# Optimization experiments

Hardware: AMD Instinct MI355X
Metric: run time of the kernel (lower is better)

Reference implementation:

```python
import jax, jax.numpy as jnp
import numpy as np

NUM_HEADS = 4
K_CLOSEST = 8
LN_EPS = 1e-5

B, N_REC, N_KP, F = 8, 4096, 20, 256


def setup_inputs() -> dict:
    key = jax.random.key(0)
    ks = jax.random.split(key, 5)
    h_rec = jax.random.normal(ks[0], (B, N_REC, F), dtype=jnp.float32)
    x_rec = jax.random.normal(ks[1], (B, N_REC, 3), dtype=jnp.float32) * 3.0
    h0_kp = jax.random.normal(ks[2], (B, N_KP, F), dtype=jnp.float32)
    # fc_src (shared for src and dst, bias=False): in_feats -> out_feats*num_heads
    W_src = jax.random.normal(ks[3], (F, F * NUM_HEADS), dtype=jnp.float32) / np.sqrt(F)
    # kp_feature_mlp: Linear(out_feats + k_closest, out_feats) + SiLU
    W_mlp = jax.random.normal(ks[4], (F + K_CLOSEST, F), dtype=jnp.float32) / np.sqrt(F + K_CLOSEST)
    b_mlp = jnp.zeros((F,), dtype=jnp.float32)
    ln_gamma = jnp.ones((F,), dtype=jnp.float32)
    ln_beta = jnp.zeros((F,), dtype=jnp.float32)
    return {"h_rec": h_rec, "x_rec": x_rec, "h0_kp": h0_kp, "W_src": W_src,
            "W_mlp": W_mlp, "b_mlp": b_mlp, "ln_gamma": ln_gamma, "ln_beta": ln_beta}


def reference(h_rec, x_rec, h0_kp, W_src, W_mlp, b_mlp, ln_gamma, ln_beta):
    Bb, Nr, Fd = h_rec.shape
    Nk = h0_kp.shape[1]
    H = NUM_HEADS
    D = W_src.shape[1] // H  # out_feats per head

    # fc_src applied to both rec and kp features (matches source, fc_dst unused)
    ft_src = (h_rec @ W_src).reshape(Bb, Nr, H, D)   # [B, Nr, H, D]
    ft_dst = (h0_kp @ W_src).reshape(Bb, Nk, H, D)   # [B, Nk, H, D]

    # per-edge dot-product scores over the complete bipartite rec->kp graph
    a = jnp.einsum('brhd,bkhd->brkh', ft_src, ft_dst) / jnp.sqrt(jnp.float32(D))
    a = jnp.exp(a)  # source uses plain exp (no max subtraction)
    sa = a / jnp.sum(a, axis=1, keepdims=True)        # segment softmax over rec atoms per kp

    # attention-weighted aggregation of rec positions, mean over heads
    agg = jnp.einsum('brkh,brc->bkhc', sa, x_rec)     # [B, Nk, H, 3]
    kp_pos = agg.mean(axis=2)                          # [B, Nk, 3]

    # k-closest rec atoms per keypoint
    x_diff = x_rec[:, None, :, :] - kp_pos[:, :, None, :]          # [B, Nk, Nr, 3]
    dist = jnp.sqrt(jnp.sum((x_diff + 1e-30) ** 2, axis=-1))       # [B, Nk, Nr]
    neg_dk, idx = jax.lax.top_k(-dist, K_CLOSEST)                  # idx: [B, Nk, K]
    d_k = -neg_dk                                                  # [B, Nk, K]

    # mean of rec features over the k nearest atoms (per-batch gather)
    h_knn = jax.vmap(lambda h, i: h[i])(h_rec, idx)                # [B, Nk, K, F]
    h_m = h_knn.mean(axis=2)                                       # [B, Nk, F]

    feat_in = jnp.concatenate([h_m, d_k], axis=-1)                 # [B, Nk, F+K]
    kp_feat = jax.nn.silu(feat_in @ W_mlp + b_mlp)

    # LayerNorm (norm=True)
    mu = kp_feat.mean(axis=-1, keepdims=True)
    var = kp_feat.var(axis=-1, keepdims=True)
    kp_feat = (kp_feat - mu) * jax.lax.rsqrt(var + LN_EPS) * ln_gamma + ln_beta
    return kp_pos, kp_feat
```

## Files before the change

### kernel.cpp

```cpp
#include <hip/hip_runtime.h>
#include <math.h>

static constexpr int NB  = 8;
static constexpr int NRC = 4096;
static constexpr int NKP = 20;
static constexpr int NF  = 256;
static constexpr int NHD = 4;
static constexpr int DD  = 256;
static constexpr int NKH = NKP * NHD;
static constexpr int KCL = 8;
static constexpr int NT  = 32;
static constexpr float SCALE = 0.0625f;

static constexpr int WT_OFF = 0;
static constexpr int M_OFF  = 262144;
static constexpr int P_OFF  = 0;

__global__ __launch_bounds__(256) void k0_transpose(const float* __restrict__ W,
                                                    float* __restrict__ WT) {
    __shared__ float tile[64][65];
    int c0 = (blockIdx.x & 15) * 64;
    int f0 = (blockIdx.x >> 4) * 64;
    int lx = threadIdx.x & 63, ly = threadIdx.x >> 6;
#pragma unroll
    for (int rr = 0; rr < 16; ++rr) {
        int fr = ly + rr * 4;
        tile[fr][lx] = W[(f0 + fr) * 1024 + c0 + lx];
    }
    __syncthreads();
#pragma unroll
    for (int rr = 0; rr < 16; ++rr) {
        int cr = ly + rr * 4;
        WT[(c0 + cr) * 256 + f0 + lx] = tile[lx][cr];
    }
}

__global__ __launch_bounds__(256) void k12_m(const float* __restrict__ h0,
                                             const float* __restrict__ W,
                                             const float* __restrict__ WT,
                                             float* __restrict__ M) {
    int bx = blockIdx.x;
    int b  = bx >> 4;
    int h  = (bx >> 2) & 3;
    int kq = bx & 3;
    int k0 = kq * 5;
    int tid = threadIdx.x;

    __shared__ float h0l[5][256];
    __shared__ float ftl[5][256];
#pragma unroll
    for (int k = 0; k < 5; ++k)
        h0l[k][tid] = h0[(b * NKP + k0 + k) * NF + tid];
    __syncthreads();

    {
        float a0 = 0.f, a1 = 0.f, a2 = 0.f, a3 = 0.f, a4 = 0.f;
        const float* wp = W + h * DD + tid;
#pragma unroll 2
        for (int g4 = 0; g4 < 64; ++g4) {
            float4 hk0 = *(const float4*)&h0l[0][g4 * 4];
            float4 hk1 = *(const float4*)&h0l[1][g4 * 4];
            float4 hk2 = *(const float4*)&h0l[2][g4 * 4];
            float4 hk3 = *(const float4*)&h0l[3][g4 * 4];
            float4 hk4 = *(const float4*)&h0l[4][g4 * 4];
#pragma unroll
            for (int j = 0; j < 4; ++j) {
                float w = wp[(g4 * 4 + j) * 1024];
                a0 += w * ((const float*)&hk0)[j];
                a1 += w * ((const float*)&hk1)[j];
                a2 += w * ((const float*)&hk2)[j];
                a3 += w * ((const float*)&hk3)[j];
                a4 += w * ((const float*)&hk4)[j];
            }
        }
        ftl[0][tid] = a0; ftl[1][tid] = a1; ftl[2][tid] = a2;
        ftl[3][tid] = a3; ftl[4][tid] = a4;
    }
    __syncthreads();

    float m0 = 0.f, m1 = 0.f, m2 = 0.f, m3 = 0.f, m4 = 0.f;
    const float* wtp = WT + (h * DD) * NF + tid;
#pragma unroll 2
    for (int d4 = 0; d4 < 64; ++d4) {
        float4 f0v = *(const float4*)&ftl[0][d4 * 4];
        float4 f1v = *(const float4*)&ftl[1][d4 * 4];
        float4 f2v = *(const float4*)&ftl[2][d4 * 4];
        float4 f3v = *(const float4*)&ftl[3][d4 * 4];
        float4 f4v = *(const float4*)&ftl[4][d4 * 4];
#pragma unroll
        for (int j = 0; j < 4; ++j) {
            float wt = wtp[(d4 * 4 + j) * 256];
            m0 += wt * ((const float*)&f0v)[j];
            m1 += wt * ((const float*)&f1v)[j];
            m2 += wt * ((const float*)&f2v)[j];
            m3 += wt * ((const float*)&f3v)[j];
            m4 += wt * ((const float*)&f4v)[j];
        }
    }
    M[(b * NKH + (k0 + 0) * NHD + h) * NF + tid] = m0 * SCALE;
    M[(b * NKH + (k0 + 1) * NHD + h) * NF + tid] = m1 * SCALE;
    M[(b * NKH + (k0 + 2) * NHD + h) * NF + tid] = m2 * SCALE;
    M[(b * NKH + (k0 + 3) * NHD + h) * NF + tid] = m3 * SCALE;
    M[(b * NKH + (k0 + 4) * NHD + h) * NF + tid] = m4 * SCALE;
}

__global__ __launch_bounds__(512) void k3_scores(const float* __restrict__ hrec,
                                                 const float* __restrict__ xrec,
                                                 const float* __restrict__ Mg,
                                                 float* __restrict__ P) {
    extern __shared__ float Ml[];
    int bx = blockIdx.x;
    int b = bx >> 5, t = bx & 31;
    int tid = threadIdx.x;

    const float4* Mg4 = (const float4*)(Mg + b * NKH * NF);
    for (int i = tid; i < NKH * NF / 4; i += 512) {
        float4 v = Mg4[i];
        int kh = i >> 6;
        int f4 = (i & 63) * 4;
        Ml[(f4 + 0) * 80 + kh] = v.x;
        Ml[(f4 + 1) * 80 + kh] = v.y;
        Ml[(f4 + 2) * 80 + kh] = v.z;
        Ml[(f4 + 3) * 80 + kh] = v.w;
    }
    __syncthreads();

    int q = tid >> 6;
    int lane = tid & 63;
    int r0 = t * 128 + lane * 2;

    float acc0[10], acc1[10];
#pragma unroll
    for (int i = 0; i < 10; ++i) { acc0[i] = 0.f; acc1[i] = 0.f; }

    const float4* ha = (const float4*)(hrec + ((size_t)b * NRC + r0) * NF);
    const float4* hb = (const float4*)(hrec + ((size_t)b * NRC + r0 + 1) * NF);

#pragma unroll 2
    for (int f4 = 0; f4 < 64; ++f4) {
        float4 va = ha[f4], vb = hb[f4];
#pragma unroll
        for (int j = 0; j < 4; ++j) {
            int f = f4 * 4 + j;
            const float2* m2 = (const float2*)(Ml + f * 80 + q * 10);
            float A = ((const float*)&va)[j];
            float B = ((const float*)&vb)[j];
#pragma unroll
            for (int c2 = 0; c2 < 5; ++c2) {
                float2 mv = m2[c2];
                acc0[c2 * 2 + 0] += A * mv.x;
                acc0[c2 * 2 + 1] += A * mv.y;
                acc1[c2 * 2 + 0] += B * mv.x;
                acc1[c2 * 2 + 1] += B * mv.y;
            }
        }
    }

    const float* xa = xrec + ((size_t)b * NRC + r0) * 3;
    float x0 = xa[0], y0 = xa[1], z0 = xa[2];
    float x1 = xa[3], y1 = xa[4], z1 = xa[5];

    float s[10][4];
#pragma unroll
    for (int c = 0; c < 10; ++c) {
        float e0 = __expf(acc0[c]);
        float e1 = __expf(acc1[c]);
        s[c][0] = e0 + e1;
        s[c][1] = e0 * x0 + e1 * x1;
        s[c][2] = e0 * y0 + e1 * y1;
        s[c][3] = e0 * z0 + e1 * z1;
    }
#pragma unroll
    for (int c = 0; c < 10; ++c)
#pragma unroll
        for (int st = 0; st < 4; ++st)
#pragma unroll
            for (int m = 1; m < 64; m <<= 1)
                s[c][st] += __shfl_xor(s[c][st], m, 64);

    if (lane == 0) {
        float* Pp = P + ((size_t)(b * NT + t) * NKH + q * 10) * 4;
#pragma unroll
        for (int c = 0; c < 10; ++c)
#pragma unroll
            for (int st = 0; st < 4; ++st)
                Pp[c * 4 + st] = s[c][st];
    }
}

__global__ __launch_bounds__(256) void k4_final(const float* __restrict__ hrec,
                                                const float* __restrict__ xrec,
                                                const float* __restrict__ P,
                                                const float* __restrict__ Wm,
                                                const float* __restrict__ bm,
                                                const float* __restrict__ gam,
                                                const float* __restrict__ bet,
                                                float* __restrict__ out) {
    int bx = blockIdx.x;
    int b = bx / NKP, k = bx % NKP;
    int tid = threadIdx.x;

    __shared__ float Sh[NHD][4];
    __shared__ float posl[3];
    __shared__ float d2[NRC];
    __shared__ float fin[NF + KCL];
    __shared__ int kidx[KCL];
    __shared__ float cd[4];
    __shared__ int ci[4];
    __shared__ float bcast[2];
    __shared__ float wred[4][2];

    if (tid < 16) {
        int h = tid >> 2, s = tid & 3;
        float a = 0.f;
#pragma unroll 4
        for (int t = 0; t < NT; ++t)
            a += P[((b * NT + t) * NKH + k * NHD + h) * 4 + s];
        Sh[h][s] = a;
    }
    __syncthreads();
    if (tid == 0) {
        for (int c = 0; c < 3; ++c) {
            float p = 0.f;
            for (int h = 0; h < NHD; ++h) p += Sh[h][c + 1] / Sh[h][0];
            p *= 0.25f;
            posl[c] = p;
            out[(b * NKP + k) * 3 + c] = p;
        }
    }
    __syncthreads();

    float px = posl[0], py = posl[1], pz = posl[2];
    for (int i = tid; i < NRC; i += 256) {
        const float* x = xrec + (size_t)(b * NRC + i) * 3;
        float dx = x[0] - px, dy = x[1] - py, dz = x[2] - pz;
        d2[i] = dx * dx + dy * dy + dz * dz;
    }
    __syncthreads();

    for (int j = 0; j < KCL; ++j) {
        float bd = 3.4e38f;
        int bi = -1;
        for (int i = tid; i < NRC; i += 256) {
            float v = d2[i];
            if (v < bd || (v == bd && i < bi)) { bd = v; bi = i; }
        }
        for (int off = 32; off >= 1; off >>= 1) {
            float od = __shfl_down(bd, off, 64);
            int oi = __shfl_down(bi, off, 64);
            if (od < bd || (od == bd && oi < bi)) { bd = od; bi = oi; }
        }
        if ((tid & 63) == 0) { cd[tid >> 6] = bd; ci[tid >> 6] = bi; }
        __syncthreads();
        if (tid == 0) {
            for (int w = 1; w < 4; ++w) {
                if (cd[w] < bd || (cd[w] == bd && ci[w] < bi)) { bd = cd[w]; bi = ci[w]; }
            }
            kidx[j] = bi;
            fin[NF + j] = sqrtf(bd);
            d2[bi] = 3.4e38f;
        }
        __syncthreads();
    }

    float hm = 0.f;
#pragma unroll
    for (int j = 0; j < KCL; ++j)
        hm += hrec[(size_t)(b * NRC + kidx[j]) * NF + tid];
    fin[tid] = hm * 0.125f;
    __syncthreads();

    float p = bm[tid];
#pragma unroll 4
    for (int i = 0; i < NF + KCL; ++i)
        p += fin[i] * Wm[i * NF + tid];
    float v = p / (1.f + __expf(-p));

    float s = v, sq = v * v;
#pragma unroll
    for (int m = 1; m < 64; m <<= 1) {
        s += __shfl_xor(s, m, 64);
        sq += __shfl_xor(sq, m, 64);
    }
    if ((tid & 63) == 0) { wred[tid >> 6][0] = s; wred[tid >> 6][1] = sq; }
    __syncthreads();
    if (tid == 0) {
        float ts = 0.f, tq = 0.f;
        for (int w = 0; w < 4; ++w) { ts += wred[w][0]; tq += wred[w][1]; }
        float mu = ts / 256.f;
        float var = tq / 256.f - mu * mu;
        bcast[0] = mu;
        bcast[1] = rsqrtf(var + 1e-5f);
    }
    __syncthreads();
    float o = (v - bcast[0]) * bcast[1] * gam[tid] + bet[tid];
    out[NB * NKP * 3 + (b * NKP + k) * NF + tid] = o;
}

extern "C" void kernel_launch(void* const* d_in, const int* in_sizes, int n_in,
                              void* d_out, int out_size, void* d_ws, size_t ws_size,
                              hipStream_t stream) {
    const float* h_rec = (const float*)d_in[0];
    const float* x_rec = (const float*)d_in[1];
    const float* h0_kp = (const float*)d_in[2];
    const float* W_src = (const float*)d_in[3];
    const float* W_mlp = (const float*)d_in[4];
    const float* b_mlp = (const float*)d_in[5];
    const float* gam   = (const float*)d_in[6];
    const float* bet   = (const float*)d_in[7];
    float* outp = (float*)d_out;
    float* ws = (float*)d_ws;

    float* WT = ws + WT_OFF;
    float* M  = ws + M_OFF;
    float* P  = ws + P_OFF;

    (void)hipFuncSetAttribute((const void*)k3_scores,
                              hipFuncAttributeMaxDynamicSharedMemorySize, 81920);

    hipLaunchKernelGGL(k0_transpose, dim3(64), dim3(256), 0, stream, W_src, WT);
    hipLaunchKernelGGL(k12_m, dim3(128), dim3(256), 0, stream, h0_kp, W_src, WT, M);
    hipLaunchKernelGGL(k3_scores, dim3(256), dim3(512), 81920, stream,
                       h_rec, x_rec, M, P);
    hipLaunchKernelGGL(k4_final, dim3(160), dim3(256), 0, stream,
                       h_rec, x_rec, P, W_mlp, b_mlp, gam, bet, outp);
}
```

Measured before the change: 195.5 us.

## Restructure all kernels: finer transpose, per-keypoint M, 4-row score tiles, register top-k

Rewrites every stage. The transpose uses smaller tiles across more blocks. The M projection runs one block per keypoint with 512 threads. The score kernel splits the 80 keypoint-heads into two groups of 40, and each thread handles 4 rows using float4 dot products against an untransposed shared M tile. The top-k selection keeps a sorted list of 8 candidates per thread in registers instead of rescanning shared memory, and the MLP's K dimension is split across two thread halves. The aim is to raise parallelism and cut reduction and scan overhead, at the cost of more register pressure and strided per-thread hrec reads in the score kernel.

Result: slower. 232.6 us (+19.0%).

```diff
diff --git a/kernel.cpp b/kernel.cpp
--- a/kernel.cpp
+++ b/kernel.cpp
@@ -6,10 +6,9 @@
 static constexpr int NKP = 20;
 static constexpr int NF  = 256;
 static constexpr int NHD = 4;
-static constexpr int DD  = 256;
 static constexpr int NKH = NKP * NHD;
 static constexpr int KCL = 8;
-static constexpr int NT  = 32;
+static constexpr int NT  = 16;
 static constexpr float SCALE = 0.0625f;
 
 static constexpr int WT_OFF = 0;
@@ -18,177 +17,149 @@
 
 __global__ __launch_bounds__(256) void k0_transpose(const float* __restrict__ W,
                                                     float* __restrict__ WT) {
-    __shared__ float tile[64][65];
+    __shared__ float tile[32][65];
     int c0 = (blockIdx.x & 15) * 64;
-    int f0 = (blockIdx.x >> 4) * 64;
+    int f0 = (blockIdx.x >> 4) * 32;
     int lx = threadIdx.x & 63, ly = threadIdx.x >> 6;
 #pragma unroll
-    for (int rr = 0; rr < 16; ++rr) {
+    for (int rr = 0; rr < 8; ++rr) {
         int fr = ly + rr * 4;
         tile[fr][lx] = W[(f0 + fr) * 1024 + c0 + lx];
     }
     __syncthreads();
-#pragma unroll
-    for (int rr = 0; rr < 16; ++rr) {
-        int cr = ly + rr * 4;
-        WT[(c0 + cr) * 256 + f0 + lx] = tile[lx][cr];
-    }
-}
-
-__global__ __launch_bounds__(256) void k12_m(const float* __restrict__ h0,
+    int lf = threadIdx.x & 31, cy = threadIdx.x >> 5;
+#pragma unroll
+    for (int rr = 0; rr < 8; ++rr) {
+        int cr = cy + rr * 8;
+        WT[(c0 + cr) * 256 + f0 + lf] = tile[lf][cr];
+    }
+}
+
+__global__ __launch_bounds__(512) void k12_m(const float* __restrict__ h0,
                                              const float* __restrict__ W,
                                              const float* __restrict__ WT,
                                              float* __restrict__ M) {
     int bx = blockIdx.x;
-    int b  = bx >> 4;
-    int h  = (bx >> 2) & 3;
-    int kq = bx & 3;
-    int k0 = kq * 5;
+    int b = bx / NKP, k = bx % NKP;
     int tid = threadIdx.x;
-
-    __shared__ float h0l[5][256];
-    __shared__ float ftl[5][256];
-#pragma unroll
-    for (int k = 0; k < 5; ++k)
-        h0l[k][tid] = h0[(b * NKP + k0 + k) * NF + tid];
-    __syncthreads();
-
+    __shared__ float h0l[NF];
+    __shared__ float ftl[1024];
+    if (tid < NF) h0l[tid] = h0[(b * NKP + k) * NF + tid];
+    __syncthreads();
     {
-        float a0 = 0.f, a1 = 0.f, a2 = 0.f, a3 = 0.f, a4 = 0.f;
-        const float* wp = W + h * DD + tid;
-#pragma unroll 2
-        for (int g4 = 0; g4 < 64; ++g4) {
-            float4 hk0 = *(const float4*)&h0l[0][g4 * 4];
-            float4 hk1 = *(const float4*)&h0l[1][g4 * 4];
-            float4 hk2 = *(const float4*)&h0l[2][g4 * 4];
-            float4 hk3 = *(const float4*)&h0l[3][g4 * 4];
-            float4 hk4 = *(const float4*)&h0l[4][g4 * 4];
-#pragma unroll
-            for (int j = 0; j < 4; ++j) {
-                float w = wp[(g4 * 4 + j) * 1024];
-                a0 += w * ((const float*)&hk0)[j];
-                a1 += w * ((const float*)&hk1)[j];
-                a2 += w * ((const float*)&hk2)[j];
-                a3 += w * ((const float*)&hk3)[j];
-                a4 += w * ((const float*)&hk4)[j];
-            }
-        }
-        ftl[0][tid] = a0; ftl[1][tid] = a1; ftl[2][tid] = a2;
-        ftl[3][tid] = a3; ftl[4][tid] = a4;
-    }
-    __syncthreads();
-
-    float m0 = 0.f, m1 = 0.f, m2 = 0.f, m3 = 0.f, m4 = 0.f;
-    const float* wtp = WT + (h * DD) * NF + tid;
-#pragma unroll 2
-    for (int d4 = 0; d4 < 64; ++d4) {
-        float4 f0v = *(const float4*)&ftl[0][d4 * 4];
-        float4 f1v = *(const float4*)&ftl[1][d4 * 4];
-        float4 f2v = *(const float4*)&ftl[2][d4 * 4];
-        float4 f3v = *(const float4*)&ftl[3][d4 * 4];
-        float4 f4v = *(const float4*)&ftl[4][d4 * 4];
-#pragma unroll
-        for (int j = 0; j < 4; ++j) {
-            float wt = wtp[(d4 * 4 + j) * 256];
-            m0 += wt * ((const float*)&f0v)[j];
-            m1 += wt * ((const float*)&f1v)[j];
-            m2 += wt * ((const float*)&f2v)[j];
-            m3 += wt * ((const float*)&f3v)[j];
-            m4 += wt * ((const float*)&f4v)[j];
-        }
-    }
-    M[(b * NKH + (k0 + 0) * NHD + h) * NF + tid] = m0 * SCALE;
-    M[(b * NKH + (k0 + 1) * NHD + h) * NF + tid] = m1 * SCALE;
-    M[(b * NKH + (k0 + 2) * NHD + h) * NF + tid] = m2 * SCALE;
-    M[(b * NKH + (k0 + 3) * NHD + h) * NF + tid] = m3 * SCALE;
-    M[(b * NKH + (k0 + 4) * NHD + h) * NF + tid] = m4 * SCALE;
+        float a0 = 0.f, a1 = 0.f;
+        const float* wp = W + tid;
+#pragma unroll 4
+        for (int g = 0; g < NF; ++g) {
+            float hg = h0l[g];
+            a0 += hg * wp[g * 1024];
+            a1 += hg * wp[g * 1024 + 512];
+        }
+        ftl[tid] = a0;
+        ftl[tid + 512] = a1;
+    }
+    __syncthreads();
+    {
+        int f = tid & 255, h = tid >> 8;
+        float a0 = 0.f, a1 = 0.f;
+        const float* wt0 = WT + (h * 256) * 256 + f;
+        const float* wt1 = WT + ((h + 2) * 256) * 256 + f;
+        const float* f0p = ftl + h * 256;
+        const float* f1p = ftl + (h + 2) * 256;
+#pragma unroll 4
+        for (int d = 0; d < 256; ++d) {
+            a0 += f0p[d] * wt0[d * 256];
+            a1 += f1p[d] * wt1[d * 256];
+        }
+        M[((size_t)b * NKH + k * NHD + h) * NF + f]     = a0 * SCALE;
+        M[((size_t)b * NKH + k * NHD + h + 2) * NF + f] = a1 * SCALE;
+    }
 }
 
 __global__ __launch_bounds__(512) void k3_scores(const float* __restrict__ hrec,
                                                  const float* __restrict__ xrec,
                                                  const float* __restrict__ Mg,
                                                  float* __restrict__ P) {
-    extern __shared__ float Ml[];
+    __shared__ float Ml[40 * 256];
     int bx = blockIdx.x;
-    int b = bx >> 5, t = bx & 31;
+    int b = bx >> 5;
+    int rem = bx & 31;
+    int t = rem >> 1;
+    int g = rem & 1;
     int tid = threadIdx.x;
 
-    const float4* Mg4 = (const float4*)(Mg + b * NKH * NF);
-    for (int i = tid; i < NKH * NF / 4; i += 512) {
-        float4 v = Mg4[i];
-        int kh = i >> 6;
-        int f4 = (i & 63) * 4;
-        Ml[(f4 + 0) * 80 + kh] = v.x;
-        Ml[(f4 + 1) * 80 + kh] = v.y;
-        Ml[(f4 + 2) * 80 + kh] = v.z;
-        Ml[(f4 + 3) * 80 + kh] = v.w;
-    }
-    __syncthreads();
-
-    int q = tid >> 6;
-    int lane = tid & 63;
-    int r0 = t * 128 + lane * 2;
-
-    float acc0[10], acc1[10];
-#pragma unroll
-    for (int i = 0; i < 10; ++i) { acc0[i] = 0.f; acc1[i] = 0.f; }
-
-    const float4* ha = (const float4*)(hrec + ((size_t)b * NRC + r0) * NF);
-    const float4* hb = (const float4*)(hrec + ((size_t)b * NRC + r0 + 1) * NF);
+    const float4* Mg4 = (const float4*)(Mg + ((size_t)b * NKH + g * 40) * NF);
+    float4* Ml4 = (float4*)Ml;
+#pragma unroll
+    for (int i = 0; i < 5; ++i)
+        Ml4[i * 512 + tid] = Mg4[i * 512 + tid];
+    __syncthreads();
+
+    int w = tid >> 6, lane = tid & 63;
+    int c0 = w * 5;
+    int r0 = t * 256 + lane * 4;
+
+    float acc[5][4];
+#pragma unroll
+    for (int c = 0; c < 5; ++c)
+#pragma unroll
+        for (int r = 0; r < 4; ++r) acc[c][r] = 0.f;
+
+    const float4* A = (const float4*)(hrec + ((size_t)b * NRC + r0) * NF);
+    const float* Mlc = Ml + c0 * NF;
 
 #pragma unroll 2
     for (int f4 = 0; f4 < 64; ++f4) {
-        float4 va = ha[f4], vb = hb[f4];
-#pragma unroll
-        for (int j = 0; j < 4; ++j) {
-            int f = f4 * 4 + j;
-            const float2* m2 = (const float2*)(Ml + f * 80 + q * 10);
-            float A = ((const float*)&va)[j];
-            float B = ((const float*)&vb)[j];
-#pragma unroll
-            for (int c2 = 0; c2 < 5; ++c2) {
-                float2 mv = m2[c2];
-                acc0[c2 * 2 + 0] += A * mv.x;
-                acc0[c2 * 2 + 1] += A * mv.y;
-                acc1[c2 * 2 + 0] += B * mv.x;
-                acc1[c2 * 2 + 1] += B * mv.y;
-            }
-        }
-    }
-
-    const float* xa = xrec + ((size_t)b * NRC + r0) * 3;
-    float x0 = xa[0], y0 = xa[1], z0 = xa[2];
-    float x1 = xa[3], y1 = xa[4], z1 = xa[5];
-
-    float s[10][4];
-#pragma unroll
-    for (int c = 0; c < 10; ++c) {
-        float e0 = __expf(acc0[c]);
-        float e1 = __expf(acc1[c]);
-        s[c][0] = e0 + e1;
-        s[c][1] = e0 * x0 + e1 * x1;
-        s[c][2] = e0 * y0 + e1 * y1;
-        s[c][3] = e0 * z0 + e1 * z1;
-    }
-#pragma unroll
-    for (int c = 0; c < 10; ++c)
-#pragma unroll
-        for (int st = 0; st < 4; ++st)
-#pragma unroll
-            for (int m = 1; m < 64; m <<= 1)
-                s[c][st] += __shfl_xor(s[c][st], m, 64);
-
-    if (lane == 0) {
-        float* Pp = P + ((size_t)(b * NT + t) * NKH + q * 10) * 4;
-#pragma unroll
-        for (int c = 0; c < 10; ++c)
-#pragma unroll
-            for (int st = 0; st < 4; ++st)
-                Pp[c * 4 + st] = s[c][st];
-    }
-}
-
-__global__ __launch_bounds__(256) void k4_final(const float* __restrict__ hrec,
+        float4 a0 = A[f4];
+        float4 a1 = A[64 + f4];
+        float4 a2 = A[128 + f4];
+        float4 a3 = A[192 + f4];
+#pragma unroll
+        for (int c = 0; c < 5; ++c) {
+            float4 m = *(const float4*)(Mlc + c * NF + f4 * 4);
+            acc[c][0] += a0.x * m.x + a0.y * m.y + a0.z * m.z + a0.w * m.w;
+            acc[c][1] += a1.x * m.x + a1.y * m.y + a1.z * m.z + a1.w * m.w;
+            acc[c][2] += a2.x * m.x + a2.y * m.y + a2.z * m.z + a2.w * m.w;
+            acc[c][3] += a3.x * m.x + a3.y * m.y + a3.z * m.z + a3.w * m.w;
+        }
+    }
+
+    const float4* X = (const float4*)(xrec + ((size_t)b * NRC + r0) * 3);
+    float4 x0 = X[0], x1 = X[1], x2 = X[2];
+    float xs[4] = {x0.x, x0.w, x1.z, x2.y};
+    float ys[4] = {x0.y, x1.x, x1.w, x2.z};
+    float zs[4] = {x0.z, x1.y, x2.x, x2.w};
+
+    float* Pp = P + ((size_t)(b * NT + t) * NKH + g * 40 + c0) * 4;
+#pragma unroll
+    for (int c = 0; c < 5; ++c) {
+        float e0 = __expf(acc[c][0]), e1 = __expf(acc[c][1]);
+        float e2 = __expf(acc[c][2]), e3 = __expf(acc[c][3]);
+        float s0 = e0 + e1 + e2 + e3;
+        float s1 = e0 * xs[0] + e1 * xs[1] + e2 * xs[2] + e3 * xs[3];
+        float s2 = e0 * ys[0] + e1 * ys[1] + e2 * ys[2] + e3 * ys[3];
+        float s3 = e0 * zs[0] + e1 * zs[1] + e2 * zs[2] + e3 * zs[3];
+#pragma unroll
+        for (int m = 1; m < 64; m <<= 1) {
+            s0 += __shfl_xor(s0, m, 64);
+            s1 += __shfl_xor(s1, m, 64);
+            s2 += __shfl_xor(s2, m, 64);
+            s3 += __shfl_xor(s3, m, 64);
+        }
+        if (lane == 0) {
+            Pp[c * 4 + 0] = s0; Pp[c * 4 + 1] = s1;
+            Pp[c * 4 + 2] = s2; Pp[c * 4 + 3] = s3;
+        }
+    }
+}
+
+#define CSWAP(i, j)                                                         \
+    if (d[j] < d[i] || (d[j] == d[i] && ix[j] < ix[i])) {                   \
+        float td = d[i]; d[i] = d[j]; d[j] = td;                            \
+        int ti = ix[i]; ix[i] = ix[j]; ix[j] = ti;                          \
+    }
+
+__global__ __launch_bounds__(512) void k4_final(const float* __restrict__ hrec,
                                                 const float* __restrict__ xrec,
                                                 const float* __restrict__ P,
                                                 const float* __restrict__ Wm,
@@ -199,30 +170,33 @@
     int bx = blockIdx.x;
     int b = bx / NKP, k = bx % NKP;
     int tid = threadIdx.x;
-
-    __shared__ float Sh[NHD][4];
-    __shared__ float posl[3];
-    __shared__ float d2[NRC];
+    int w = tid >> 6, lane = tid & 63;
+
+    __shared__ float Sh[16];
+    __shared__ float posl[4];
+    __shared__ float redv[8];
+    __shared__ int   redi[8];
+    __shared__ int   kidxs[KCL];
     __shared__ float fin[NF + KCL];
-    __shared__ int kidx[KCL];
-    __shared__ float cd[4];
-    __shared__ int ci[4];
-    __shared__ float bcast[2];
-    __shared__ float wred[4][2];
+    __shared__ float part[2][NF];
+    __shared__ float wred[8][2];
+    __shared__ float stat[2];
 
     if (tid < 16) {
         int h = tid >> 2, s = tid & 3;
         float a = 0.f;
-#pragma unroll 4
+#pragma unroll
         for (int t = 0; t < NT; ++t)
             a += P[((b * NT + t) * NKH + k * NHD + h) * 4 + s];
-        Sh[h][s] = a;
+        Sh[tid] = a;
     }
     __syncthreads();
     if (tid == 0) {
+#pragma unroll
         for (int c = 0; c < 3; ++c) {
             float p = 0.f;
-            for (int h = 0; h < NHD; ++h) p += Sh[h][c + 1] / Sh[h][0];
+#pragma unroll
+            for (int h = 0; h < NHD; ++h) p += Sh[h * 4 + c + 1] / Sh[h * 4];
             p *= 0.25f;
             posl[c] = p;
             out[(b * NKP + k) * 3 + c] = p;
@@ -231,70 +205,96 @@
     __syncthreads();
 
     float px = posl[0], py = posl[1], pz = posl[2];
-    for (int i = tid; i < NRC; i += 256) {
-        const float* x = xrec + (size_t)(b * NRC + i) * 3;
+    float d[8];
+    int ix[8];
+#pragma unroll
+    for (int s = 0; s < 8; ++s) {
+        int i = s * 512 + tid;
+        const float* x = xrec + ((size_t)b * NRC + i) * 3;
         float dx = x[0] - px, dy = x[1] - py, dz = x[2] - pz;
-        d2[i] = dx * dx + dy * dy + dz * dz;
-    }
-    __syncthreads();
+        d[s] = dx * dx + dy * dy + dz * dz;
+        ix[s] = i;
+    }
+    CSWAP(0, 1) CSWAP(2, 3) CSWAP(4, 5) CSWAP(6, 7)
+    CSWAP(0, 2) CSWAP(1, 3) CSWAP(4, 6) CSWAP(5, 7)
+    CSWAP(1, 2) CSWAP(5, 6)
+    CSWAP(0, 4) CSWAP(1, 5) CSWAP(2, 6) CSWAP(3, 7)
+    CSWAP(2, 4) CSWAP(3, 5)
+    CSWAP(1, 2) CSWAP(3, 4) CSWAP(5, 6)
 
     for (int j = 0; j < KCL; ++j) {
-        float bd = 3.4e38f;
-        int bi = -1;
-        for (int i = tid; i < NRC; i += 256) {
-            float v = d2[i];
-            if (v < bd || (v == bd && i < bi)) { bd = v; bi = i; }
-        }
-        for (int off = 32; off >= 1; off >>= 1) {
-            float od = __shfl_down(bd, off, 64);
-            int oi = __shfl_down(bi, off, 64);
+        float bd = d[0];
+        int bi = ix[0];
+#pragma unroll
+        for (int m = 1; m < 64; m <<= 1) {
+            float od = __shfl_xor(bd, m, 64);
+            int oi = __shfl_xor(bi, m, 64);
             if (od < bd || (od == bd && oi < bi)) { bd = od; bi = oi; }
         }
-        if ((tid & 63) == 0) { cd[tid >> 6] = bd; ci[tid >> 6] = bi; }
+        if (lane == 0) { redv[w] = bd; redi[w] = bi; }
         __syncthreads();
-        if (tid == 0) {
-            for (int w = 1; w < 4; ++w) {
-                if (cd[w] < bd || (cd[w] == bd && ci[w] < bi)) { bd = cd[w]; bi = ci[w]; }
-            }
-            kidx[j] = bi;
-            fin[NF + j] = sqrtf(bd);
-            d2[bi] = 3.4e38f;
+        bd = redv[0]; bi = redi[0];
+#pragma unroll
+        for (int q = 1; q < 8; ++q) {
+            float od = redv[q]; int oi = redi[q];
+            if (od < bd || (od == bd && oi < bi)) { bd = od; bi = oi; }
+        }
+        if (tid == 0) { kidxs[j] = bi; fin[NF + j] = sqrtf(bd); }
+        if (ix[0] == bi) {
+#pragma unroll
+            for (int s = 0; s < 7; ++s) { d[s] = d[s + 1]; ix[s] = ix[s + 1]; }
+            d[7] = 3.4e38f; ix[7] = 0x7fffffff;
         }
         __syncthreads();
     }
 
-    float hm = 0.f;
-#pragma unroll
-    for (int j = 0; j < KCL; ++j)
-        hm += hrec[(size_t)(b * NRC + kidx[j]) * NF + tid];
-    fin[tid] = hm * 0.125f;
-    __syncthreads();
-
-    float p = bm[tid];
-#pragma unroll 4
-    for (int i = 0; i < NF + KCL; ++i)
-        p += fin[i] * Wm[i * NF + tid];
-    float v = p / (1.f + __expf(-p));
-
+    if (tid < NF) {
+        float hm = 0.f;
+#pragma unroll
+        for (int j = 0; j < KCL; ++j)
+            hm += hrec[((size_t)b * NRC + kidxs[j]) * NF + tid];
+        fin[tid] = hm * 0.125f;
+    }
+    __syncthreads();
+
+    {
+        int o = tid & 255, p = tid >> 8;
+        float acc = 0.f;
+        const float* wp = Wm + o;
+#pragma unroll 2
+        for (int i = p * 132; i < p * 132 + 132; ++i)
+            acc += fin[i] * wp[i * NF];
+        part[p][o] = acc;
+    }
+    __syncthreads();
+
+    float v = 0.f;
+    if (tid < NF) {
+        float psum = bm[tid] + part[0][tid] + part[1][tid];
+        v = psum / (1.f + __expf(-psum));
+    }
     float s = v, sq = v * v;
 #pragma unroll
     for (int m = 1; m < 64; m <<= 1) {
         s += __shfl_xor(s, m, 64);
         sq += __shfl_xor(sq, m, 64);
     }
-    if ((tid & 63) == 0) { wred[tid >> 6][0] = s; wred[tid >> 6][1] = sq; }
+    if (lane == 0) { wred[w][0] = s; wred[w][1] = sq; }
     __syncthreads();
     if (tid == 0) {
         float ts = 0.f, tq = 0.f;
-        for (int w = 0; w < 4; ++w) { ts += wred[w][0]; tq += wred[w][1]; }
+#pragma unroll
+        for (int q = 0; q < 8; ++q) { ts += wred[q][0]; tq += wred[q][1]; }
         float mu = ts / 256.f;
         float var = tq / 256.f - mu * mu;
-        bcast[0] = mu;
-        bcast[1] = rsqrtf(var + 1e-5f);
-    }
-    __syncthreads();
-    float o = (v - bcast[0]) * bcast[1] * gam[tid] + bet[tid];
-    out[NB * NKP * 3 + (b * NKP + k) * NF + tid] = o;
+        stat[0] = mu;
+        stat[1] = rsqrtf(var + 1e-5f);
+    }
+    __syncthreads();
+    if (tid < NF) {
+        float o = (v - stat[0]) * stat[1] * gam[tid] + bet[tid];
+        out[NB * NKP * 3 + (b * NKP + k) * NF + tid] = o;
+    }
 }
 
 extern "C" void kernel_launch(void* const* d_in, const int* in_sizes, int n_in,
@@ -315,13 +315,10 @@
     float* M  = ws + M_OFF;
     float* P  = ws + P_OFF;
 
-    (void)hipFuncSetAttribute((const void*)k3_scores,
-                              hipFuncAttributeMaxDynamicSharedMemorySize, 81920);
-
-    hipLaunchKernelGGL(k0_transpose, dim3(64), dim3(256), 0, stream, W_src, WT);
-    hipLaunchKernelGGL(k12_m, dim3(128), dim3(256), 0, stream, h0_kp, W_src, WT, M);
-    hipLaunchKernelGGL(k3_scores, dim3(256), dim3(512), 81920, stream,
+    hipLaunchKernelGGL(k0_transpose, dim3(128), dim3(256), 0, stream, W_src, WT);
+    hipLaunchKernelGGL(k12_m, dim3(160), dim3(512), 0, stream, h0_kp, W_src, WT, M);
+    hipLaunchKernelGGL(k3_scores, dim3(256), dim3(512), 0, stream,
                        h_rec, x_rec, M, P);
-    hipLaunchKernelGGL(k4_final, dim3(160), dim3(256), 0, stream,
+    hipLaunchKernelGGL(k4_final, dim3(160), dim3(512), 0, stream,
                        h_rec, x_rec, P, W_mlp, b_mlp, gam, bet, outp);
 }
```
